# Performance work log

Hardware: AMD Instinct MI355X
Metric: run time of the kernel (lower is better)

## Reference

```python
import jax, jax.numpy as jnp
import numpy as np

M = 8      # bits // 8 experts
SUB = 8    # sub-code width per expert
HID = 256  # expert output classes (2**SUB)
BITS = 64
NCLS = 100
NUM_FLIP = (BITS // 32) ** 2  # 4


def _bit_flip(x, template, key):
    # torch: rand.argsort(-1) -> shuffledTemplate = template[idx]; x[mask] *= -1
    rand = jax.random.uniform(key, x.shape)
    idx = jnp.argsort(rand, axis=-1)
    mask = template[idx]
    return jnp.where(mask, -x, x)


def _map_net(x, W1, b1, W2, b2):
    # m independent Linear(8,256)->SiLU->Linear(256,256) experts over contiguous chunks
    N = x.shape[0]
    xs = x.reshape(N, M, SUB)
    h = jax.nn.silu(jnp.einsum('nmi,mih->nmh', xs, W1) + b1)
    return jnp.einsum('nmh,mho->nmo', h, W2) + b2  # [N, M, HID]


def setup_inputs() -> dict:
    key = jax.random.key(0)
    ks = jax.random.split(key, 10)
    N = 32768
    x = jax.random.normal(ks[0], (N, BITS), jnp.float32)
    # multi-label targets, guarantee >=1 positive per row (meanWeight divides by row sum)
    y = (jax.random.uniform(ks[1], (N, NCLS)) < 0.1).astype(jnp.int32)
    lab = jax.random.randint(ks[2], (N,), 0, NCLS)
    y = y.at[jnp.arange(N), lab].set(1)
    centroids = (jax.random.uniform(ks[3], (NCLS, BITS)) > 0.5).astype(jnp.float32)
    permIdx = jax.random.permutation(ks[4], BITS)

    def make_template(k):
        t = jnp.zeros(BITS, bool).at[:NUM_FLIP].set(True)
        return jax.random.permutation(k, t)

    template_map = make_template(ks[5])
    template_raw = make_template(ks[6])
    W1 = jax.random.normal(ks[7], (M, SUB, HID), jnp.float32) / np.sqrt(SUB)
    b1 = jnp.zeros((M, HID), jnp.float32)
    W2 = jax.random.normal(ks[8], (M, HID, HID), jnp.float32) / np.sqrt(HID)
    b2 = jnp.zeros((M, HID), jnp.float32)
    return dict(x=x, y=y, centroids=centroids, permIdx=permIdx,
                template_map=template_map, template_raw=template_raw,
                W1=W1, b1=b1, W2=W2, b2=b2)


def reference(x, y, centroids, permIdx, template_map, template_raw, W1, b1, W2, b2):
    N = x.shape[0]
    multiplier = 2 ** jnp.arange(SUB)  # [8]
    kmap, kraw = jax.random.split(jax.random.key(1))

    xp = x[:, permIdx]  # permuted codes [N, BITS]
    x_det = jax.lax.stop_gradient(xp)

    # ---- mapLoss path (x detached; mapper params still trained; dropout in eval) ----
    logits_map = _map_net(_bit_flip(x_det, template_map, kmap), W1, b1, W2, b2)  # [N,M,HID]
    raw_flipped = _bit_flip(x_det, template_raw, kraw)
    binary = raw_flipped.reshape(N, M, SUB) > 0
    target = (binary * multiplier).sum(-1)  # [N, M] decimal sub-codes
    lse = jax.nn.logsumexp(logits_map, axis=-1)
    picked = jnp.take_along_axis(logits_map, target[..., None], axis=-1)[..., 0]
    mapLoss = (lse - picked).mean(0).sum()  # sum over m of per-chunk CE means
    hitRate = (logits_map.argmax(-1) == target).astype(jnp.float32).mean()

    # ---- netLoss path (mapper on non-detached x, no flip; centers detached) ----
    hashCenter = jax.lax.stop_gradient(centroids[:, permIdx])  # [C, BITS]
    centerBits = hashCenter > 0
    centerTarget = (centerBits.reshape(NCLS, M, SUB) * multiplier).sum(-1)  # [C, M]
    logits_net = _map_net(xp, W1, b1, W2, b2)  # [N, M, HID]
    lse2 = jax.nn.logsumexp(logits_net, axis=-1)  # [N, M]
    # picked2[n,m,c] = logits_net[n, m, centerTarget[c, m]]
    picked2 = logits_net[:, jnp.arange(M)[:, None], centerTarget.T]  # [N, M, C]
    ce = lse2[..., None] - picked2  # [N, M, C]
    mask = y > 0
    w = mask.astype(jnp.float32)
    w = w / w.sum(-1, keepdims=True)  # meanWeight (mask * meanWeight == meanWeight)
    netLoss = (ce * w[:, None, :]).sum() / N

    # ---- codes-to-center Hamming distance, masked mean over (n, c) with y>0 ----
    xb = (xp > 0).astype(jnp.float32)
    cb = centerBits.astype(jnp.float32)
    ham = xb.sum(-1, keepdims=True) + cb.sum(-1)[None, :] - 2.0 * (xb @ cb.T)  # [N, C]
    mf = mask.astype(jnp.float32)
    codesToCenterDistance = (ham * mf).sum() / mf.sum()

    total = netLoss + mapLoss
    return (total, netLoss, mapLoss, hitRate, codesToCenterDistance)
```

## Files before the change

kernel.cpp:

```cpp
#include <hip/hip_runtime.h>
#include <stdint.h>

#define NR 32768
#define MM 8
#define NCLS 100
#define HALFN 1048576u
#define HSS 260
#define LGS 260
#define PSS 12

#define LOG2E 1.4426950408889634f
#define LN2F  0.6931471805599453f

typedef _Float16 h8 __attribute__((ext_vector_type(8)));
typedef _Float16 h4 __attribute__((ext_vector_type(4)));
typedef float f4 __attribute__((ext_vector_type(4)));
typedef unsigned long long ull;

__host__ __device__ inline void tf2x32(uint32_t k0, uint32_t k1, uint32_t x0, uint32_t x1,
                                       uint32_t& o0, uint32_t& o1) {
  uint32_t ks0 = k0, ks1 = k1, ks2 = k0 ^ k1 ^ 0x1BD11BDAu;
  x0 += ks0; x1 += ks1;
#define TFR(r) { x0 += x1; x1 = (x1 << r) | (x1 >> (32 - r)); x1 ^= x0; }
  TFR(13) TFR(15) TFR(26) TFR(6)  x0 += ks1; x1 += ks2 + 1u;
  TFR(17) TFR(29) TFR(16) TFR(24) x0 += ks2; x1 += ks0 + 2u;
  TFR(13) TFR(15) TFR(26) TFR(6)  x0 += ks0; x1 += ks1 + 3u;
  TFR(17) TFR(29) TFR(16) TFR(24) x0 += ks1; x1 += ks2 + 4u;
  TFR(13) TFR(15) TFR(26) TFR(6)  x0 += ks2; x1 += ks0 + 5u;
#undef TFR
  o0 = x0; o1 = x1;
}

__device__ inline int load_tmpl(const void* p, int lane) {
  const unsigned* pi = (const unsigned*)p;
  unsigned w = pi[lane];
  ull okF = __ballot(w == 0u || w == 0x3F800000u);
  ull onF = __ballot(w == 0x3F800000u);
  ull okI = __ballot(w <= 1u);
  ull onI = __ballot(w == 1u);
  if (okF == ~0ull && __popcll(onF) == 4) return (w == 0x3F800000u) ? 1 : 0;
  if (okI == ~0ull && __popcll(onI) == 4) return (int)w;
  const unsigned char* pb = (const unsigned char*)p;
  return pb[lane] ? 1 : 0;
}

__device__ inline uint32_t packh2(float a, float b) {
  union { _Float16 h[2]; uint32_t u; } cv;
  cv.h[0] = (_Float16)a; cv.h[1] = (_Float16)b;
  return cv.u;
}

__device__ inline ull flip_mask(ull tmask, uint32_t key) {
  ull fm = 0;
  while (tmask) {
    int p = __ffsll((long long)tmask) - 1;
    tmask &= tmask - 1;
    uint32_t kp = (uint32_t)__builtin_amdgcn_readlane((int)key, p);
    fm |= 1ull << __popcll(__ballot(key < kp));
  }
  return fm;
}

__global__ __launch_bounds__(256) void stage1p(
    const float* __restrict__ x, const int* __restrict__ y, const int* __restrict__ perm,
    const void* tmap, const void* traw,
    uint32_t km0, uint32_t km1, uint32_t kr0, uint32_t kr1,
    const float* __restrict__ W2, const float* __restrict__ W1,
    const float* __restrict__ B1, const float* __restrict__ B2,
    const float* __restrict__ centroids,
    _Float16* __restrict__ Wp, _Float16* __restrict__ Wp1, float* __restrict__ B2s,
    ull* __restrict__ cb64,
    uint32_t* __restrict__ xp16, uint32_t* __restrict__ xm16,
    ull* __restrict__ targ, ull* __restrict__ xb,
    float* __restrict__ winv, unsigned char* __restrict__ poslist, int* __restrict__ nposA) {
  int b = blockIdx.x, tid = threadIdx.x;
  if (b >= 2048) {
    int pb = b - 2048;
    if (pb < 256) {
      int gid = pb * 256 + tid;
      int lane6 = gid & 63, frag = gid >> 6;
      int NT = frag & 15, kt = (frag >> 4) & 7, m = frag >> 7;
      int q = lane6 >> 4, lr = lane6 & 15;
      const float* src = W2 + (size_t)m * 65536 + (size_t)(kt * 32 + q * 8) * 256 + NT * 16 + lr;
      h8 v;
#pragma unroll
      for (int j = 0; j < 8; j++) v[j] = (_Float16)src[j * 256];
      *(h8*)(Wp + (size_t)gid * 8) = v;
    } else if (pb < 288) {
      int idx = (pb - 256) * 256 + tid;
      int lane = idx & 63, t = (idx >> 6) & 15, m = idx >> 10;
      int q = lane >> 4, lr = lane & 15;
      h8 v;
#pragma unroll
      for (int j = 0; j < 8; j++) {
        float val = 0.0f;
        if (q == 0) val = W1[(size_t)(m * 8 + j) * 256 + t * 16 + lr] * LOG2E;
        else if (q == 1 && j == 0) val = B1[m * 256 + t * 16 + lr] * LOG2E;
        v[j] = (_Float16)val;
      }
      *(h8*)(Wp1 + (size_t)idx * 8) = v;
    } else if (pb < 313) {
      int c = (pb - 288) * 4 + (tid >> 6);
      int lane = tid & 63;
      ull bits = __ballot(centroids[c * 64 + perm[lane]] > 0.0f);
      if (lane == 0 && c < NCLS) cb64[c] = bits;
    } else {
#pragma unroll
      for (int j = 0; j < 8; j++) B2s[tid * 8 + j] = B2[tid * 8 + j] * LOG2E;
    }
    return;
  }

  int wv = tid >> 6, lane = tid & 63;
  int tm = load_tmpl(tmap, lane);
  int tr = load_tmpl(traw, lane);
  ull tmm = __ballot(tm != 0);
  ull trm = __ballot(tr != 0);
  int pv = perm[lane];

  int nbase = b * 8 + wv * 2;
  uint32_t bmv[4], brv[4];
  {
    uint32_t iA = (uint32_t)(nbase * 64 + lane);
    uint32_t iB = iA + 64u;
    tf2x32(km0, km1, iA, iA + HALFN, bmv[0], bmv[2]);
    tf2x32(kr0, kr1, iA, iA + HALFN, brv[0], brv[2]);
    tf2x32(km0, km1, iB, iB + HALFN, bmv[1], bmv[3]);
    tf2x32(kr0, kr1, iB, iB + HALFN, brv[1], brv[3]);
  }
  const int nn[4] = {nbase, nbase + 1, nbase + 16384, nbase + 16385};
  float xr[4];
  int yv1[4], yv2[4];
#pragma unroll
  for (int rr = 0; rr < 4; rr++) {
    int n = nn[rr];
    xr[rr] = x[(size_t)n * 64 + pv];
    yv1[rr] = y[(size_t)n * NCLS + lane];
    yv2[rr] = (lane < NCLS - 64) ? y[(size_t)n * NCLS + 64 + lane] : 0;
  }
#pragma unroll
  for (int rr = 0; rr < 4; rr++) {
    int n = nn[rr];
    float xpv = xr[rr];
    uint32_t kmk = ((bmv[rr] >> 9) << 6) | (uint32_t)lane;
    uint32_t krk = ((brv[rr] >> 9) << 6) | (uint32_t)lane;
    ull fm = flip_mask(tmm, kmk);
    ull fr = flip_mask(trm, krk);
    float xmv = ((fm >> lane) & 1ull) ? -xpv : xpv;
    float rfv = ((fr >> lane) & 1ull) ? -xpv : xpv;
    float xp_o = __shfl_xor(xpv, 1);
    float xm_o = __shfl_xor(xmv, 1);
    if ((lane & 1) == 0) {
      xp16[n * 32 + (lane >> 1)] = packh2(xpv, xp_o);
      xm16[n * 32 + (lane >> 1)] = packh2(xmv, xm_o);
    }
    ull t64 = __ballot(rfv > 0.0f);
    ull b64v = __ballot(xpv > 0.0f);

    int c1 = yv1[rr] > 0;
    int c2 = yv2[rr] > 0;
    ull p0 = __ballot(c1);
    ull p1 = __ballot(c2);
    int cnt0 = __popcll(p0);
    float cnt = (float)(cnt0 + __popcll(p1));

    unsigned char* pl = poslist + (size_t)n * 64;
    ull below = (lane == 0) ? 0ull : (~0ull >> (64 - lane));
    if (c1) pl[__popcll(p0 & below)] = (unsigned char)lane;
    if (c2) pl[cnt0 + __popcll(p1 & below)] = (unsigned char)(64 + lane);

    if (lane == 0) {
      targ[n] = t64;
      xb[n] = b64v;
      winv[n] = 1.0f / cnt;
      nposA[n] = cnt0 + __popcll(p1);
    }
  }
}

__global__ __launch_bounds__(512, 8) void mapnet8(
    const uint32_t* __restrict__ Xm16, const uint32_t* __restrict__ Xp16,
    const _Float16* __restrict__ Wp1, const _Float16* __restrict__ Wp,
    const float* __restrict__ B2s,
    const ull* __restrict__ targ, const float* __restrict__ winv,
    const unsigned char* __restrict__ poslist, const int* __restrict__ nposA,
    const ull* __restrict__ cb64, const ull* __restrict__ xb,
    float* __restrict__ accbuf) {
  __shared__ union {
    _Float16 h[64 * HSS];
    float lg[32 * LGS];
  } u;
  __shared__ float ps[64 * PSS];
  __shared__ float pm[64 * PSS];
  __shared__ float mvA[64];
  __shared__ int   tA[64];
  __shared__ float sl[6];
  const int tid = threadIdx.x, lane = tid & 63, wv = tid >> 6;
  const int q = lane >> 4, lr = lane & 15;
  const int m = blockIdx.y, pass = blockIdx.z;
  const int n0 = blockIdx.x * 64;
  if (tid < 6) sl[tid] = 0.0f;

  const uint32_t* Xin = pass ? Xp16 : Xm16;
  const bool doHam = (pass == 0) && (m == 0);

  float hamS = 0.0f, npS = 0.0f;
  if (doHam) {
    ull xv[8];
    int np[8];
    unsigned char pc[8];
    const int nh = n0 + wv * 8;
#pragma unroll
    for (int r = 0; r < 8; r++) {
      xv[r] = xb[nh + r];
      np[r] = nposA[nh + r];
      pc[r] = poslist[(size_t)(nh + r) * 64 + lane];
    }
#pragma unroll
    for (int r = 0; r < 8; r++) {
      if (lane < np[r]) {
        ull cb = cb64[pc[r]];
        hamS += (float)__popcll(xv[r]) + (float)__popcll(cb) - 2.0f * (float)__popcll(xv[r] & cb);
      }
      npS += (float)np[r];
    }
#pragma unroll
    for (int off = 1; off < 64; off <<= 1) hamS += __shfl_xor(hamS, off);
  }

  const int rb = wv & 3, tbase = (wv >> 2) * 8;
  h8 af;
  {
    const _Float16* xsrc = (const _Float16*)(Xin + (size_t)(n0 + rb * 16 + lr) * 32) + m * 8;
    h8 xv = *(const h8*)xsrc;
    h8 zero = {(_Float16)0.0f, (_Float16)0.0f, (_Float16)0.0f, (_Float16)0.0f,
               (_Float16)0.0f, (_Float16)0.0f, (_Float16)0.0f, (_Float16)0.0f};
    af = (q == 0) ? xv : zero;
    if (q == 1) af[0] = (_Float16)1.0f;
  }
#pragma unroll 4
  for (int tt = 0; tt < 8; tt++) {
    int t = tbase + tt;
    h8 wfrag = *(const h8*)(Wp1 + ((size_t)(m * 16 + t) * 64 + lane) * 8);
    f4 z = __builtin_amdgcn_mfma_f32_16x16x32_f16(wfrag, af, (f4){0.f, 0.f, 0.f, 0.f}, 0, 0, 0);
    h4 pk;
#pragma unroll
    for (int reg = 0; reg < 4; reg++) {
      float z2 = z[reg];
      pk[reg] = (_Float16)(z2 * __builtin_amdgcn_rcpf(1.0f + __builtin_amdgcn_exp2f(-z2)));
    }
    *(h4*)(u.h + (size_t)(rb * 16 + lr) * HSS + t * 16 + q * 4) = pk;
  }
  __syncthreads();

  f4 acc4[4][2];
  {
    f4 bv0 = *(const f4*)(B2s + m * 256 + wv * 32 + q * 4);
    f4 bv1 = *(const f4*)(B2s + m * 256 + wv * 32 + 16 + q * 4);
#pragma unroll
    for (int rt = 0; rt < 4; rt++) { acc4[rt][0] = bv0; acc4[rt][1] = bv1; }
  }
  const size_t wbase = (size_t)m * 65536;
#pragma unroll 2
  for (int kt = 0; kt < 8; kt++) {
    h8 bh0 = *(const h8*)(Wp + wbase + (((size_t)kt * 16 + wv * 2 + 0) * 64 + lane) * 8);
    h8 bh1 = *(const h8*)(Wp + wbase + (((size_t)kt * 16 + wv * 2 + 1) * 64 + lane) * 8);
#pragma unroll
    for (int rt = 0; rt < 4; rt++) {
      const _Float16* p = u.h + (size_t)(rt * 16 + lr) * HSS + kt * 32 + q * 8;
      h4 lo = *(const h4*)p;
      h4 hi = *(const h4*)(p + 4);
      h8 ah = __builtin_shufflevector(lo, hi, 0, 1, 2, 3, 4, 5, 6, 7);
      acc4[rt][0] = __builtin_amdgcn_mfma_f32_16x16x32_f16(bh0, ah, acc4[rt][0], 0, 0, 0);
      acc4[rt][1] = __builtin_amdgcn_mfma_f32_16x16x32_f16(bh1, ah, acc4[rt][1], 0, 0, 0);
    }
  }

  float rsum[4], rmax[4];
#pragma unroll
  for (int rt = 0; rt < 4; rt++) {
    f4 l0 = acc4[rt][0], l1 = acc4[rt][1];
    float s = 0.0f;
#pragma unroll
    for (int reg = 0; reg < 4; reg++)
      s += __builtin_amdgcn_exp2f(l0[reg]) + __builtin_amdgcn_exp2f(l1[reg]);
    rsum[rt] = s;
    if (pass == 0) {
      float mv = fmaxf(l0[0], l1[0]);
#pragma unroll
      for (int reg = 1; reg < 4; reg++) mv = fmaxf(mv, fmaxf(l0[reg], l1[reg]));
      rmax[rt] = mv;
    }
  }
#pragma unroll
  for (int rt = 0; rt < 4; rt++) {
    rsum[rt] += __shfl_xor(rsum[rt], 16);
    rsum[rt] += __shfl_xor(rsum[rt], 32);
  }
  if (pass == 0) {
#pragma unroll
    for (int rt = 0; rt < 4; rt++) {
      rmax[rt] = fmaxf(rmax[rt], __shfl_xor(rmax[rt], 16));
      rmax[rt] = fmaxf(rmax[rt], __shfl_xor(rmax[rt], 32));
    }
  }
  if (lane < 16) {
#pragma unroll
    for (int rt = 0; rt < 4; rt++) {
      ps[(rt * 16 + lane) * PSS + wv] = rsum[rt];
      if (pass == 0) pm[(rt * 16 + lane) * PSS + wv] = rmax[rt];
    }
  }

  if (pass == 0) {
    __syncthreads();
    float myLse = 0.0f;
    if (tid < 64) {
      int row = tid, n = n0 + row;
      f4 s0 = *(const f4*)(ps + row * PSS);
      f4 s1 = *(const f4*)(ps + row * PSS + 4);
      f4 ss = s0 + s1;
      float s = (ss[0] + ss[1]) + (ss[2] + ss[3]);
      f4 m0 = *(const f4*)(pm + row * PSS);
      f4 m1 = *(const f4*)(pm + row * PSS + 4);
      float mv = fmaxf(fmaxf(fmaxf(m0[0], m0[1]), fmaxf(m0[2], m0[3])),
                       fmaxf(fmaxf(m1[0], m1[1]), fmaxf(m1[2], m1[3])));
      mvA[row] = mv;
      tA[row] = (int)((targ[n] >> (m * 8)) & 0xFFull);
      myLse = __builtin_amdgcn_logf(s);
    }
    __syncthreads();
    float pick = 0.0f, hit = 0.0f;
    const int cbase = wv * 32 + q * 4;
#pragma unroll
    for (int rt = 0; rt < 4; rt++) {
      int row = rt * 16 + lr;
      int d0 = tA[row] - cbase;
#pragma unroll
      for (int nt = 0; nt < 2; nt++) {
        int d = d0 - nt * 16;
        if ((unsigned)d < 4u) {
          f4 f = acc4[rt][nt];
          float v = f[0];
          v = (d == 1) ? f[1] : v;
          v = (d == 2) ? f[2] : v;
          v = (d == 3) ? f[3] : v;
          pick += v;
          hit += (v == mvA[row]) ? 1.0f : 0.0f;
        }
      }
    }
    float lossC = myLse - pick;
#pragma unroll
    for (int off = 1; off < 64; off <<= 1) {
      lossC += __shfl_xor(lossC, off);
      hit += __shfl_xor(hit, off);
    }
    if (lane == 0) {
      atomicAdd(&sl[0], lossC);
      atomicAdd(&sl[2], hit);
      if (doHam) {
        atomicAdd(&sl[3], hamS);
        atomicAdd(&sl[4], npS);
      }
    }
  } else {
    float partLoss = 0.0f;
    for (int ph = 0; ph < 2; ph++) {
      __syncthreads();
#pragma unroll
      for (int rt2 = 0; rt2 < 2; rt2++) {
#pragma unroll
        for (int nt = 0; nt < 2; nt++)
#pragma unroll
          for (int reg = 0; reg < 4; reg++)
            u.lg[(rt2 * 16 + lr) * LGS + wv * 32 + nt * 16 + q * 4 + reg] =
                acc4[ph * 2 + rt2][nt][reg];
      }
      __syncthreads();
      int rl = tid >> 4;
      int grow = ph * 32 + rl;
      int n = n0 + grow;
      int cl = tid & 15;
      const float* lrow = u.lg + rl * LGS;
      int np = nposA[n];
      const unsigned char* pl = poslist + (size_t)n * 64;
      float sp = 0.0f;
      for (int j2 = cl; j2 < np; j2 += 16) {
        int c = pl[j2];
        int t = (int)((cb64[c] >> (m * 8)) & 0xFFull);
        sp += lrow[t];
      }
#pragma unroll
      for (int off = 1; off < 16; off <<= 1) sp += __shfl_xor(sp, off);
      if (cl == 0) {
        f4 s0 = *(const f4*)(ps + grow * PSS);
        f4 s1 = *(const f4*)(ps + grow * PSS + 4);
        f4 ss = s0 + s1;
        float s = (ss[0] + ss[1]) + (ss[2] + ss[3]);
        partLoss += __builtin_amdgcn_logf(s) - winv[n] * sp;
      }
    }
    partLoss += __shfl_xor(partLoss, 16);
    partLoss += __shfl_xor(partLoss, 32);
    if (lane == 0) atomicAdd(&sl[1], partLoss);
  }

  __syncthreads();
  if (tid == 0) {
    float* slot = accbuf + (blockIdx.x & 127) * 8;
    if (pass == 0) {
      atomicAdd(&slot[0], sl[0]);
      atomicAdd(&slot[2], sl[2]);
      if (doHam) {
        atomicAdd(&slot[3], sl[3]);
        atomicAdd(&slot[4], sl[4]);
      }
    } else {
      atomicAdd(&slot[1], sl[1]);
    }
  }
}

__global__ __launch_bounds__(128) void finalk(const float* __restrict__ accbuf, float* __restrict__ out) {
  int t = threadIdx.x;
  float v0 = accbuf[t * 8 + 0], v1 = accbuf[t * 8 + 1], v2 = accbuf[t * 8 + 2];
  float v3 = accbuf[t * 8 + 3], v4 = accbuf[t * 8 + 4];
#pragma unroll
  for (int off = 1; off < 64; off <<= 1) {
    v0 += __shfl_xor(v0, off); v1 += __shfl_xor(v1, off); v2 += __shfl_xor(v2, off);
    v3 += __shfl_xor(v3, off); v4 += __shfl_xor(v4, off);
  }
  __shared__ float s[2][5];
  if ((t & 63) == 0) {
    s[t >> 6][0] = v0; s[t >> 6][1] = v1; s[t >> 6][2] = v2; s[t >> 6][3] = v3; s[t >> 6][4] = v4;
  }
  __syncthreads();
  if (t == 0) {
    float a0 = s[0][0] + s[1][0], a1 = s[0][1] + s[1][1], a2 = s[0][2] + s[1][2];
    float a3 = s[0][3] + s[1][3], a4 = s[0][4] + s[1][4];
    float netLoss = a1 * LN2F / (float)NR;
    float mapLoss = a0 * LN2F / (float)NR;
    out[0] = netLoss + mapLoss;
    out[1] = netLoss;
    out[2] = mapLoss;
    out[3] = a2 / (float)(NR * MM);
    out[4] = a3 / a4;
  }
}

extern "C" void kernel_launch(void* const* d_in, const int* in_sizes, int n_in,
                              void* d_out, int out_size, void* d_ws, size_t ws_size,
                              hipStream_t stream) {
  const float* x = (const float*)d_in[0];
  const int* y = (const int*)d_in[1];
  const float* centroids = (const float*)d_in[2];
  const int* perm = (const int*)d_in[3];
  const void* tmap = d_in[4];
  const void* traw = d_in[5];
  const float* W1 = (const float*)d_in[6];
  const float* B1 = (const float*)d_in[7];
  const float* W2 = (const float*)d_in[8];
  const float* B2 = (const float*)d_in[9];
  float* out = (float*)d_out;

  char* w = (char*)d_ws;
  float* accbuf = (float*)w;
  uint32_t* xp16 = (uint32_t*)(w + 4096);
  uint32_t* xm16 = xp16 + (size_t)NR * 32;
  ull* targ = (ull*)(xm16 + (size_t)NR * 32);
  ull* cb64 = targ + NR;
  ull* xb = cb64 + 128;
  float* winv = (float*)(xb + NR);
  int* nposA = (int*)(winv + NR);
  unsigned char* poslist = (unsigned char*)(nposA + NR);
  _Float16* Wp = (_Float16*)(poslist + (size_t)NR * 64);
  _Float16* Wp1 = Wp + (1 << 19);
  float* B2s = (float*)(Wp1 + (1 << 16));

  hipMemsetAsync(accbuf, 0, 4096, stream);

  uint32_t a0, b0, a1, b1;
  tf2x32(0u, 1u, 0u, 2u, a0, b0);
  tf2x32(0u, 1u, 1u, 3u, a1, b1);

  stage1p<<<2048 + 314, 256, 0, stream>>>(x, y, perm, tmap, traw, a0, a1, b0, b1,
                                          W2, W1, B1, B2, centroids, Wp, Wp1, B2s, cb64,
                                          xp16, xm16, targ, xb, winv, poslist, nposA);
  dim3 g(NR / 64, MM, 2);
  mapnet8<<<g, 512, 0, stream>>>(xm16, xp16, Wp1, Wp, B2s, targ, winv, poslist, nposA,
                                 cb64, xb, accbuf);
  finalk<<<1, 128, 0, stream>>>(accbuf, out);
}
```

Baseline: 212.0 us.

## Retile second-layer GEMM to 2x4 warp tiles and relax launch bounds

Each wave of the second expert matmul now covers 32 rows by 64 output columns instead of 64 rows by 32 columns. That halves the LDS A-fragment reads per wave while doubling the global weight-fragment loads, and reuses each weight fragment across two row tiles. The row-sum and row-max partials are reduced over 4 column groups instead of 8, and the pass-1 logits write-back is split by row half. The launch-bounds occupancy hint drops from 8 to 6, which gives the compiler more registers at the cost of fewer resident waves.

```diff
diff --git a/kernel.cpp b/kernel.cpp
--- a/kernel.cpp
+++ b/kernel.cpp
@@ -178,7 +178,7 @@
   }
 }
 
-__global__ __launch_bounds__(512, 8) void mapnet8(
+__global__ __launch_bounds__(512, 6) void mapnet8(
     const uint32_t* __restrict__ Xm16, const uint32_t* __restrict__ Xp16,
     const _Float16* __restrict__ Wp1, const _Float16* __restrict__ Wp,
     const float* __restrict__ B2s,
@@ -253,62 +253,68 @@
   }
   __syncthreads();
 
-  f4 acc4[4][2];
-  {
-    f4 bv0 = *(const f4*)(B2s + m * 256 + wv * 32 + q * 4);
-    f4 bv1 = *(const f4*)(B2s + m * 256 + wv * 32 + 16 + q * 4);
-#pragma unroll
-    for (int rt = 0; rt < 4; rt++) { acc4[rt][0] = bv0; acc4[rt][1] = bv1; }
+  const int cg = wv & 3, rh = wv >> 2;
+  f4 acc4[2][4];
+#pragma unroll
+  for (int nt = 0; nt < 4; nt++) {
+    f4 bv = *(const f4*)(B2s + m * 256 + cg * 64 + nt * 16 + q * 4);
+    acc4[0][nt] = bv;
+    acc4[1][nt] = bv;
   }
   const size_t wbase = (size_t)m * 65536;
 #pragma unroll 2
   for (int kt = 0; kt < 8; kt++) {
-    h8 bh0 = *(const h8*)(Wp + wbase + (((size_t)kt * 16 + wv * 2 + 0) * 64 + lane) * 8);
-    h8 bh1 = *(const h8*)(Wp + wbase + (((size_t)kt * 16 + wv * 2 + 1) * 64 + lane) * 8);
-#pragma unroll
-    for (int rt = 0; rt < 4; rt++) {
-      const _Float16* p = u.h + (size_t)(rt * 16 + lr) * HSS + kt * 32 + q * 8;
+    h8 ah[2];
+#pragma unroll
+    for (int rt = 0; rt < 2; rt++) {
+      const _Float16* p = u.h + (size_t)(rh * 32 + rt * 16 + lr) * HSS + kt * 32 + q * 8;
       h4 lo = *(const h4*)p;
       h4 hi = *(const h4*)(p + 4);
-      h8 ah = __builtin_shufflevector(lo, hi, 0, 1, 2, 3, 4, 5, 6, 7);
-      acc4[rt][0] = __builtin_amdgcn_mfma_f32_16x16x32_f16(bh0, ah, acc4[rt][0], 0, 0, 0);
-      acc4[rt][1] = __builtin_amdgcn_mfma_f32_16x16x32_f16(bh1, ah, acc4[rt][1], 0, 0, 0);
-    }
-  }
-
-  float rsum[4], rmax[4];
-#pragma unroll
-  for (int rt = 0; rt < 4; rt++) {
-    f4 l0 = acc4[rt][0], l1 = acc4[rt][1];
+      ah[rt] = __builtin_shufflevector(lo, hi, 0, 1, 2, 3, 4, 5, 6, 7);
+    }
+#pragma unroll
+    for (int nt = 0; nt < 4; nt++) {
+      h8 bh = *(const h8*)(Wp + wbase + (((size_t)kt * 16 + cg * 4 + nt) * 64 + lane) * 8);
+      acc4[0][nt] = __builtin_amdgcn_mfma_f32_16x16x32_f16(bh, ah[0], acc4[0][nt], 0, 0, 0);
+      acc4[1][nt] = __builtin_amdgcn_mfma_f32_16x16x32_f16(bh, ah[1], acc4[1][nt], 0, 0, 0);
+    }
+  }
+
+  float rsum[2], rmax[2];
+#pragma unroll
+  for (int rt = 0; rt < 2; rt++) {
     float s = 0.0f;
 #pragma unroll
-    for (int reg = 0; reg < 4; reg++)
-      s += __builtin_amdgcn_exp2f(l0[reg]) + __builtin_amdgcn_exp2f(l1[reg]);
+    for (int nt = 0; nt < 4; nt++)
+#pragma unroll
+      for (int reg = 0; reg < 4; reg++) s += __builtin_amdgcn_exp2f(acc4[rt][nt][reg]);
     rsum[rt] = s;
     if (pass == 0) {
-      float mv = fmaxf(l0[0], l1[0]);
-#pragma unroll
-      for (int reg = 1; reg < 4; reg++) mv = fmaxf(mv, fmaxf(l0[reg], l1[reg]));
+      float mv = acc4[rt][0][0];
+#pragma unroll
+      for (int nt = 0; nt < 4; nt++)
+#pragma unroll
+        for (int reg = 0; reg < 4; reg++) mv = fmaxf(mv, acc4[rt][nt][reg]);
       rmax[rt] = mv;
     }
   }
 #pragma unroll
-  for (int rt = 0; rt < 4; rt++) {
+  for (int rt = 0; rt < 2; rt++) {
     rsum[rt] += __shfl_xor(rsum[rt], 16);
     rsum[rt] += __shfl_xor(rsum[rt], 32);
   }
   if (pass == 0) {
 #pragma unroll
-    for (int rt = 0; rt < 4; rt++) {
+    for (int rt = 0; rt < 2; rt++) {
       rmax[rt] = fmaxf(rmax[rt], __shfl_xor(rmax[rt], 16));
       rmax[rt] = fmaxf(rmax[rt], __shfl_xor(rmax[rt], 32));
     }
   }
   if (lane < 16) {
 #pragma unroll
-    for (int rt = 0; rt < 4; rt++) {
-      ps[(rt * 16 + lane) * PSS + wv] = rsum[rt];
-      if (pass == 0) pm[(rt * 16 + lane) * PSS + wv] = rmax[rt];
+    for (int rt = 0; rt < 2; rt++) {
+      ps[(rh * 32 + rt * 16 + lane) * PSS + cg] = rsum[rt];
+      if (pass == 0) pm[(rh * 32 + rt * 16 + lane) * PSS + cg] = rmax[rt];
     }
   }
 
@@ -318,26 +324,22 @@
     if (tid < 64) {
       int row = tid, n = n0 + row;
       f4 s0 = *(const f4*)(ps + row * PSS);
-      f4 s1 = *(const f4*)(ps + row * PSS + 4);
-      f4 ss = s0 + s1;
-      float s = (ss[0] + ss[1]) + (ss[2] + ss[3]);
+      float s = (s0[0] + s0[1]) + (s0[2] + s0[3]);
       f4 m0 = *(const f4*)(pm + row * PSS);
-      f4 m1 = *(const f4*)(pm + row * PSS + 4);
-      float mv = fmaxf(fmaxf(fmaxf(m0[0], m0[1]), fmaxf(m0[2], m0[3])),
-                       fmaxf(fmaxf(m1[0], m1[1]), fmaxf(m1[2], m1[3])));
+      float mv = fmaxf(fmaxf(m0[0], m0[1]), fmaxf(m0[2], m0[3]));
       mvA[row] = mv;
       tA[row] = (int)((targ[n] >> (m * 8)) & 0xFFull);
       myLse = __builtin_amdgcn_logf(s);
     }
     __syncthreads();
     float pick = 0.0f, hit = 0.0f;
-    const int cbase = wv * 32 + q * 4;
-#pragma unroll
-    for (int rt = 0; rt < 4; rt++) {
-      int row = rt * 16 + lr;
+    const int cbase = cg * 64 + q * 4;
+#pragma unroll
+    for (int rt = 0; rt < 2; rt++) {
+      int row = rh * 32 + rt * 16 + lr;
       int d0 = tA[row] - cbase;
 #pragma unroll
-      for (int nt = 0; nt < 2; nt++) {
+      for (int nt = 0; nt < 4; nt++) {
         int d = d0 - nt * 16;
         if ((unsigned)d < 4u) {
           f4 f = acc4[rt][nt];
@@ -368,14 +370,14 @@
     float partLoss = 0.0f;
     for (int ph = 0; ph < 2; ph++) {
       __syncthreads();
-#pragma unroll
-      for (int rt2 = 0; rt2 < 2; rt2++) {
-#pragma unroll
-        for (int nt = 0; nt < 2; nt++)
-#pragma unroll
-          for (int reg = 0; reg < 4; reg++)
-            u.lg[(rt2 * 16 + lr) * LGS + wv * 32 + nt * 16 + q * 4 + reg] =
-                acc4[ph * 2 + rt2][nt][reg];
+      if (rh == ph) {
+#pragma unroll
+        for (int rt = 0; rt < 2; rt++)
+#pragma unroll
+          for (int nt = 0; nt < 4; nt++)
+#pragma unroll
+            for (int reg = 0; reg < 4; reg++)
+              u.lg[(rt * 16 + lr) * LGS + cg * 64 + nt * 16 + q * 4 + reg] = acc4[rt][nt][reg];
       }
       __syncthreads();
       int rl = tid >> 4;
@@ -395,9 +397,7 @@
       for (int off = 1; off < 16; off <<= 1) sp += __shfl_xor(sp, off);
       if (cl == 0) {
         f4 s0 = *(const f4*)(ps + grow * PSS);
-        f4 s1 = *(const f4*)(ps + grow * PSS + 4);
-        f4 ss = s0 + s1;
-        float s = (ss[0] + ss[1]) + (ss[2] + ss[3]);
+        float s = (s0[0] + s0[1]) + (s0[2] + s0[3]);
         partLoss += __builtin_amdgcn_logf(s) - winv[n] * sp;
       }
     }
```

Result: slower. 226.4 us (+6.8%).
